# Kernel tuning notes

Measured on AMD Instinct MI355X. Metric: run time of the kernel, lower is better.

## Reference

```python
import jax, jax.numpy as jnp
import numpy as np

EPS = 1e-6

def _rmsnorm(x, w):
    # matches RMSNorm: compute in fp32, cast back, then scale by weight
    dt = x.dtype
    xf = x.astype(jnp.float32)
    var = jnp.mean(xf * xf, axis=-1, keepdims=True)
    xf = xf * jax.lax.rsqrt(var + EPS)
    return xf.astype(dt) * w


def setup_inputs() -> dict:
    key = jax.random.key(0)
    ks = jax.random.split(key, 4)
    B, N, C = 4, 2048, 1024
    H = 16
    D = C // H
    x = jax.random.normal(ks[0], (B, N, C), dtype=jnp.float32)
    W_qkv = jax.random.normal(ks[1], (C, 3 * C), dtype=jnp.float32) * (1.0 / np.sqrt(C))
    b_qkv = jnp.zeros((3 * C,), dtype=jnp.float32)
    W_proj = jax.random.normal(ks[2], (C, C), dtype=jnp.float32) * (1.0 / np.sqrt(C))
    b_proj = jnp.zeros((C,), dtype=jnp.float32)
    qn_w = jnp.ones((D,), dtype=jnp.float32)
    kn_w = jnp.ones((D,), dtype=jnp.float32)
    return {"x": x, "W_qkv": W_qkv, "b_qkv": b_qkv, "W_proj": W_proj,
            "b_proj": b_proj, "qn_w": qn_w, "kn_w": kn_w}


def reference(x, W_qkv, b_qkv, W_proj, b_proj, qn_w, kn_w):
    B, N, C = x.shape
    H = 16
    D = C // H
    qkv = jnp.einsum('bnc,cd->bnd', x, W_qkv) + b_qkv          # [B,N,3C]
    qkv = qkv.reshape(B, N, 3, H, D)
    q = qkv[:, :, 0].transpose(0, 2, 1, 3)                     # [B,H,N,D]
    k = qkv[:, :, 1].transpose(0, 2, 1, 3)
    v = qkv[:, :, 2].transpose(0, 2, 1, 3)
    q = _rmsnorm(q, qn_w)
    k = _rmsnorm(k, kn_w)
    scale = D ** -0.5
    attn = jnp.einsum('bhqd,bhkd->bhqk', q, k) * scale         # [B,H,N,N]
    attn = jax.nn.softmax(attn, axis=-1)
    out = jnp.einsum('bhqk,bhkd->bhqd', attn, v)               # [B,H,N,D]
    out = out.transpose(0, 2, 1, 3).reshape(B, N, C)
    out = jnp.einsum('bnc,cd->bnd', out, W_proj) + b_proj
    return out
```

## Files before the change

kernel.cpp:

```cpp
#include <hip/hip_runtime.h>
#include <stdint.h>

#define B_ 4
#define N_ 2048
#define C_ 1024
#define H_ 16
#define D_ 64
#define M_ (B_*N_)
#define N3_ (3*C_)

typedef __attribute__((ext_vector_type(8))) __bf16 bf16x8;
typedef bf16x8 bf16x8_ma __attribute__((may_alias));
typedef __attribute__((ext_vector_type(4))) float floatx4;
typedef unsigned short u16;
typedef unsigned int u32;

typedef __attribute__((address_space(1))) const void void_g;
typedef __attribute__((address_space(3))) void void_l;

__device__ __forceinline__ void glds16(const void* g, void* l) {
  __builtin_amdgcn_global_load_lds((void_g*)g, (void_l*)l, 16, 0, 0);
}

__device__ __forceinline__ u16 f2bf(float f) {
  union { float f; u32 u; } x; x.f = f;
  u32 r = x.u + 0x7fffu + ((x.u >> 16) & 1u);
  return (u16)(r >> 16);
}

__device__ __forceinline__ float fexp2(float x) {
#if __has_builtin(__builtin_amdgcn_exp2f)
  return __builtin_amdgcn_exp2f(x);
#else
  return exp2f(x);
#endif
}

__global__ __launch_bounds__(256)
void convert_x(const float4* __restrict__ in, uint2* __restrict__ out, int n4) {
  int idx = blockIdx.x * 256 + threadIdx.x;
  if (idx >= n4) return;
  float4 v = in[idx];
  union { u16 a[4]; uint2 u; } p;
  p.a[0] = f2bf(v.x); p.a[1] = f2bf(v.y); p.a[2] = f2bf(v.z); p.a[3] = f2bf(v.w);
  out[idx] = p.u;
}

__global__ __launch_bounds__(256)
void transpose_cvt(const float* __restrict__ in, u16* __restrict__ out,
                   int R, int Ccols) {
  __shared__ u16 tile[64][65];
  int c0 = blockIdx.x * 64, r0 = blockIdx.y * 64;
  int tid = threadIdx.x;
#pragma unroll
  for (int it = 0; it < 16; ++it) {
    int idx = it * 256 + tid;
    int r = idx >> 6, c = idx & 63;
    tile[c][r] = f2bf(in[(size_t)(r0 + r) * Ccols + c0 + c]);
  }
  __syncthreads();
#pragma unroll
  for (int it = 0; it < 16; ++it) {
    int idx = it * 256 + tid;
    int oc = idx >> 6, orr = idx & 63;
    out[(size_t)(c0 + oc) * R + r0 + orr] = tile[oc][orr];
  }
}

__global__ __launch_bounds__(256)
void transpose_v(const u16* __restrict__ qkv, u16* __restrict__ vt) {
  __shared__ u16 tile[64][65];
  int bh = blockIdx.y, b = bh >> 4, h = bh & 15;
  int n0 = blockIdx.x * 64;
  int tid = threadIdx.x;
#pragma unroll
  for (int it = 0; it < 16; ++it) {
    int idx = it * 256 + tid;
    int n = idx >> 6, d = idx & 63;
    tile[d][n] = qkv[(size_t)(b * N_ + n0 + n) * N3_ + 2 * C_ + h * D_ + d];
  }
  __syncthreads();
#pragma unroll
  for (int it = 0; it < 16; ++it) {
    int idx = it * 256 + tid;
    int d = idx >> 6, n = idx & 63;
    int np = (n & 0x23) | ((n & 0x0C) << 1) | ((n & 0x10) >> 2);
    vt[(size_t)(bh * D_ + d) * N_ + n0 + np] = tile[d][n];
  }
}

__global__ __launch_bounds__(256)
void gemm_bt(const u16* __restrict__ A, const u16* __restrict__ Bt,
             const float* __restrict__ bias, void* __restrict__ Cout,
             int Ncols, int lda, int do_rms, int out_fp32,
             const float* __restrict__ qn, const float* __restrict__ kn) {
  __shared__ __align__(16) u16 sA[8 * 512];
  __shared__ __align__(16) u16 sB[8 * 512];
  const int K = C_;
  int tid = threadIdx.x;
  int wave = tid >> 6, lane = tid & 63;
  int lrow = lane & 15, lq = lane >> 4;
  int n0 = blockIdx.x * 128;
  int m0 = blockIdx.y * 128;
  int wm = wave >> 1, wn = wave & 1;

  floatx4 acc[4][4];
#pragma unroll
  for (int i = 0; i < 4; ++i)
#pragma unroll
    for (int j = 0; j < 4; ++j) acc[i][j] = (floatx4){0.f, 0.f, 0.f, 0.f};

  const u16* ga0 = A  + (size_t)(m0 + (2 * wave + 0) * 16 + lrow) * lda + lq * 8;
  const u16* ga1 = A  + (size_t)(m0 + (2 * wave + 1) * 16 + lrow) * lda + lq * 8;
  const u16* gb0 = Bt + (size_t)(n0 + (2 * wave + 0) * 16 + lrow) * K + lq * 8;
  const u16* gb1 = Bt + (size_t)(n0 + (2 * wave + 1) * 16 + lrow) * K + lq * 8;
  u16* la0 = sA + (2 * wave + 0) * 512;
  u16* la1 = sA + (2 * wave + 1) * 512;
  u16* lb0 = sB + (2 * wave + 0) * 512;
  u16* lb1 = sB + (2 * wave + 1) * 512;

  for (int kt = 0; kt < K; kt += 32) {
    glds16(ga0 + kt, la0);
    glds16(ga1 + kt, la1);
    glds16(gb0 + kt, lb0);
    glds16(gb1 + kt, lb1);
    __syncthreads();
    bf16x8 af[4], bfr[4];
#pragma unroll
    for (int i = 0; i < 4; ++i)
      af[i] = *(const bf16x8_ma*)(sA + (wm * 4 + i) * 512 + lane * 8);
#pragma unroll
    for (int j = 0; j < 4; ++j)
      bfr[j] = *(const bf16x8_ma*)(sB + (wn * 4 + j) * 512 + lane * 8);
#pragma unroll
    for (int i = 0; i < 4; ++i)
#pragma unroll
      for (int j = 0; j < 4; ++j)
        acc[i][j] = __builtin_amdgcn_mfma_f32_16x16x32_bf16(af[i], bfr[j], acc[i][j], 0, 0, 0);
    __syncthreads();
  }

  int colbase = n0 + wn * 64;
  float bv[4];
#pragma unroll
  for (int j = 0; j < 4; ++j) bv[j] = bias[colbase + j * 16 + lrow];
#pragma unroll
  for (int i = 0; i < 4; ++i)
#pragma unroll
    for (int j = 0; j < 4; ++j)
#pragma unroll
      for (int r = 0; r < 4; ++r) acc[i][j][r] += bv[j];

  int sect = colbase >> 10;
  if (do_rms && sect < 2) {
    const float* wptr = (sect == 0) ? qn : kn;
    float wv[4];
#pragma unroll
    for (int j = 0; j < 4; ++j) wv[j] = wptr[j * 16 + lrow];
#pragma unroll
    for (int i = 0; i < 4; ++i)
#pragma unroll
      for (int r = 0; r < 4; ++r) {
        float ss = 0.f;
#pragma unroll
        for (int j = 0; j < 4; ++j) { float v = acc[i][j][r]; ss += v * v; }
        ss += __shfl_xor(ss, 1);
        ss += __shfl_xor(ss, 2);
        ss += __shfl_xor(ss, 4);
        ss += __shfl_xor(ss, 8);
        float rstd = rsqrtf(ss * (1.0f / 64.0f) + 1e-6f);
#pragma unroll
        for (int j = 0; j < 4; ++j) acc[i][j][r] *= rstd * wv[j];
      }
  }

#pragma unroll
  for (int i = 0; i < 4; ++i)
#pragma unroll
    for (int j = 0; j < 4; ++j)
#pragma unroll
      for (int r = 0; r < 4; ++r) {
        int row = m0 + wm * 64 + i * 16 + lq * 4 + r;
        int col = colbase + j * 16 + lrow;
        if (out_fp32)
          ((float*)Cout)[(size_t)row * Ncols + col] = acc[i][j][r];
        else
          ((u16*)Cout)[(size_t)row * Ncols + col] = f2bf(acc[i][j][r]);
      }
}

__global__ __launch_bounds__(256)
void flash_attn(u16* __restrict__ qkv, const u16* __restrict__ vt) {
  __shared__ __align__(16) u16 sK[8 * 512];
  __shared__ __align__(16) u16 sV[8 * 512];
  int tid = threadIdx.x;
  int wave = tid >> 6, lane = tid & 63;
  int lrow = lane & 15, lq = lane >> 4;
  int bh = blockIdx.y, b = bh >> 4, h = bh & 15;
  int q0 = blockIdx.x * 128;
  const float cc = 0.125f * 1.44269504088896340736f;
  const float co = 8.5f * 1.44269504088896340736f;

  bf16x8 qf[2][2];
#pragma unroll
  for (int i = 0; i < 2; ++i)
#pragma unroll
    for (int kq = 0; kq < 2; ++kq)
      qf[i][kq] = *(const bf16x8_ma*)(qkv +
          (size_t)(b * N_ + q0 + wave * 32 + i * 16 + lrow) * N3_ +
          h * D_ + kq * 32 + lq * 8);

  floatx4 aco[2][4];
#pragma unroll
  for (int i = 0; i < 2; ++i)
#pragma unroll
    for (int nd = 0; nd < 4; ++nd) aco[i][nd] = (floatx4){0.f, 0.f, 0.f, 0.f};
  float lsum[2] = {0.f, 0.f};

  for (int kt = 0; kt < 32; ++kt) {
    int key0 = kt * 64;
#pragma unroll
    for (int t = 0; t < 2; ++t) {
      int blk = wave * 2 + t;
      int j = blk >> 1, kq = blk & 1;
      const u16* g = qkv + (size_t)(b * N_ + key0 + j * 16 + lrow) * N3_ +
                     C_ + h * D_ + kq * 32 + lq * 8;
      glds16(g, sK + blk * 512);
    }
#pragma unroll
    for (int t = 0; t < 2; ++t) {
      int blk = wave * 2 + t;
      int nd = blk >> 1, kq = blk & 1;
      const u16* g = vt + (size_t)(bh * D_ + nd * 16 + lrow) * N_ +
                     key0 + kq * 32 + lq * 8;
      glds16(g, sV + blk * 512);
    }
    __syncthreads();

    floatx4 accs[2][4];
#pragma unroll
    for (int j = 0; j < 4; ++j) {
      bf16x8 kf0 = *(const bf16x8_ma*)(sK + (j * 2 + 0) * 512 + lane * 8);
      bf16x8 kf1 = *(const bf16x8_ma*)(sK + (j * 2 + 1) * 512 + lane * 8);
#pragma unroll
      for (int i = 0; i < 2; ++i) {
        floatx4 s = (floatx4){0.f, 0.f, 0.f, 0.f};
        s = __builtin_amdgcn_mfma_f32_16x16x32_bf16(kf0, qf[i][0], s, 0, 0, 0);
        s = __builtin_amdgcn_mfma_f32_16x16x32_bf16(kf1, qf[i][1], s, 0, 0, 0);
        accs[i][j] = s;
      }
    }

    bf16x8 pf[2][2];
#pragma unroll
    for (int i = 0; i < 2; ++i) {
      union { bf16x8 v; __bf16 e[8]; } pk0, pk1;
      float ls = 0.f;
#pragma unroll
      for (int j = 0; j < 4; ++j)
#pragma unroll
        for (int r = 0; r < 4; ++r) {
          float p = fexp2(fmaf(accs[i][j][r], cc, -co));
          ls += p;
          if (j < 2) pk0.e[(j & 1) * 4 + r] = (__bf16)p;
          else       pk1.e[(j & 1) * 4 + r] = (__bf16)p;
        }
      lsum[i] += ls;
      pf[i][0] = pk0.v;
      pf[i][1] = pk1.v;
    }

#pragma unroll
    for (int kq = 0; kq < 2; ++kq)
#pragma unroll
      for (int nd = 0; nd < 4; ++nd) {
        bf16x8 vf = *(const bf16x8_ma*)(sV + (nd * 2 + kq) * 512 + lane * 8);
        aco[0][nd] = __builtin_amdgcn_mfma_f32_16x16x32_bf16(vf, pf[0][kq], aco[0][nd], 0, 0, 0);
        aco[1][nd] = __builtin_amdgcn_mfma_f32_16x16x32_bf16(vf, pf[1][kq], aco[1][nd], 0, 0, 0);
      }
    __syncthreads();
  }

#pragma unroll
  for (int i = 0; i < 2; ++i) {
    float l = lsum[i];
    l += __shfl_xor(l, 16);
    l += __shfl_xor(l, 32);
    float inv = 1.0f / l;
    int row = q0 + wave * 32 + i * 16 + lrow;
#pragma unroll
    for (int nd = 0; nd < 4; ++nd) {
      union { u16 a[4]; uint2 u; } st;
#pragma unroll
      for (int r = 0; r < 4; ++r) st.a[r] = f2bf(aco[i][nd][r] * inv);
      *(uint2*)(qkv + (size_t)(b * N_ + row) * N3_ + h * D_ + nd * 16 + lq * 4) = st.u;
    }
  }
}

extern "C" void kernel_launch(void* const* d_in, const int* in_sizes, int n_in,
                              void* d_out, int out_size, void* d_ws, size_t ws_size,
                              hipStream_t stream) {
  (void)in_sizes; (void)n_in; (void)out_size; (void)ws_size;
  const float* x     = (const float*)d_in[0];
  const float* Wqkv  = (const float*)d_in[1];
  const float* bqkv  = (const float*)d_in[2];
  const float* Wproj = (const float*)d_in[3];
  const float* bproj = (const float*)d_in[4];
  const float* qn    = (const float*)d_in[5];
  const float* kn    = (const float*)d_in[6];
  float* out = (float*)d_out;

  char* ws = (char*)d_ws;
  u16* xb      = (u16*)ws;  ws += (size_t)M_ * C_ * 2;
  u16* Wt_qkv  = (u16*)ws;  ws += (size_t)N3_ * C_ * 2;
  u16* Wt_proj = (u16*)ws;  ws += (size_t)C_ * C_ * 2;
  u16* qkv     = (u16*)ws;  ws += (size_t)M_ * N3_ * 2;
  u16* vt      = (u16*)ws;  ws += (size_t)B_ * H_ * D_ * N_ * 2;

  convert_x<<<dim3(M_ * C_ / 4 / 256), 256, 0, stream>>>(
      (const float4*)x, (uint2*)xb, M_ * C_ / 4);
  transpose_cvt<<<dim3(N3_ / 64, C_ / 64), 256, 0, stream>>>(Wqkv, Wt_qkv, C_, N3_);
  transpose_cvt<<<dim3(C_ / 64, C_ / 64), 256, 0, stream>>>(Wproj, Wt_proj, C_, C_);
  gemm_bt<<<dim3(N3_ / 128, M_ / 128), 256, 0, stream>>>(
      xb, Wt_qkv, bqkv, qkv, N3_, C_, 1, 0, qn, kn);
  transpose_v<<<dim3(N_ / 64, B_ * H_), 256, 0, stream>>>(qkv, vt);
  flash_attn<<<dim3(N_ / 128, B_ * H_), 256, 0, stream>>>(qkv, vt);
  gemm_bt<<<dim3(C_ / 128, M_ / 128), 256, 0, stream>>>(
      qkv, Wt_proj, bproj, out, C_, N3_, 0, 1, qn, kn);
}
```

Measured before the change: 362.0 us.

## Double-buffer K/V tiles in flash attention and compute row sums via MFMA

```diff
diff --git a/kernel.cpp b/kernel.cpp
--- a/kernel.cpp
+++ b/kernel.cpp
@@ -191,8 +191,8 @@
 
 __global__ __launch_bounds__(256)
 void flash_attn(u16* __restrict__ qkv, const u16* __restrict__ vt) {
-  __shared__ __align__(16) u16 sK[8 * 512];
-  __shared__ __align__(16) u16 sV[8 * 512];
+  __shared__ __align__(16) u16 sK[2][8 * 512];
+  __shared__ __align__(16) u16 sV[2][8 * 512];
   int tid = threadIdx.x;
   int wave = tid >> 6, lane = tid & 63;
   int lrow = lane & 15, lq = lane >> 4;
@@ -210,38 +210,59 @@
           (size_t)(b * N_ + q0 + wave * 32 + i * 16 + lrow) * N3_ +
           h * D_ + kq * 32 + lq * 8);
 
+  union { bf16x8 v; u16 e[8]; } one_;
+#pragma unroll
+  for (int e = 0; e < 8; ++e) one_.e[e] = 0x3F80;
+  bf16x8 onef = one_.v;
+
   floatx4 aco[2][4];
-#pragma unroll
-  for (int i = 0; i < 2; ++i)
+  floatx4 acl[2];
+#pragma unroll
+  for (int i = 0; i < 2; ++i) {
 #pragma unroll
     for (int nd = 0; nd < 4; ++nd) aco[i][nd] = (floatx4){0.f, 0.f, 0.f, 0.f};
-  float lsum[2] = {0.f, 0.f};
+    acl[i] = (floatx4){0.f, 0.f, 0.f, 0.f};
+  }
+
+  const u16* gk[2];
+  const u16* gv[2];
+#pragma unroll
+  for (int t = 0; t < 2; ++t) {
+    int blk = wave * 2 + t;
+    int j = blk >> 1, kq = blk & 1;
+    gk[t] = qkv + (size_t)(b * N_ + j * 16 + lrow) * N3_ +
+            C_ + h * D_ + kq * 32 + lq * 8;
+    gv[t] = vt + (size_t)(bh * D_ + j * 16 + lrow) * N_ + kq * 32 + lq * 8;
+  }
+
+  u16* k_cur = &sK[0][0]; u16* k_nxt = &sK[1][0];
+  u16* v_cur = &sV[0][0]; u16* v_nxt = &sV[1][0];
+
+#pragma unroll
+  for (int t = 0; t < 2; ++t) {
+    int blk = wave * 2 + t;
+    glds16(gk[t], k_cur + blk * 512);
+    glds16(gv[t], v_cur + blk * 512);
+  }
+  __syncthreads();
 
   for (int kt = 0; kt < 32; ++kt) {
-    int key0 = kt * 64;
-#pragma unroll
-    for (int t = 0; t < 2; ++t) {
-      int blk = wave * 2 + t;
-      int j = blk >> 1, kq = blk & 1;
-      const u16* g = qkv + (size_t)(b * N_ + key0 + j * 16 + lrow) * N3_ +
-                     C_ + h * D_ + kq * 32 + lq * 8;
-      glds16(g, sK + blk * 512);
-    }
-#pragma unroll
-    for (int t = 0; t < 2; ++t) {
-      int blk = wave * 2 + t;
-      int nd = blk >> 1, kq = blk & 1;
-      const u16* g = vt + (size_t)(bh * D_ + nd * 16 + lrow) * N_ +
-                     key0 + kq * 32 + lq * 8;
-      glds16(g, sV + blk * 512);
-    }
-    __syncthreads();
+    if (kt < 31) {
+      size_t key0n = (size_t)(kt + 1) * 64;
+#pragma unroll
+      for (int t = 0; t < 2; ++t) {
+        int blk = wave * 2 + t;
+        glds16(gk[t] + key0n * N3_, k_nxt + blk * 512);
+        glds16(gv[t] + key0n, v_nxt + blk * 512);
+      }
+    }
 
     floatx4 accs[2][4];
+    __builtin_amdgcn_s_setprio(1);
 #pragma unroll
     for (int j = 0; j < 4; ++j) {
-      bf16x8 kf0 = *(const bf16x8_ma*)(sK + (j * 2 + 0) * 512 + lane * 8);
-      bf16x8 kf1 = *(const bf16x8_ma*)(sK + (j * 2 + 1) * 512 + lane * 8);
+      bf16x8 kf0 = *(const bf16x8_ma*)(k_cur + (j * 2 + 0) * 512 + lane * 8);
+      bf16x8 kf1 = *(const bf16x8_ma*)(k_cur + (j * 2 + 1) * 512 + lane * 8);
 #pragma unroll
       for (int i = 0; i < 2; ++i) {
         floatx4 s = (floatx4){0.f, 0.f, 0.f, 0.f};
@@ -250,43 +271,46 @@
         accs[i][j] = s;
       }
     }
+    __builtin_amdgcn_s_setprio(0);
 
     bf16x8 pf[2][2];
 #pragma unroll
     for (int i = 0; i < 2; ++i) {
       union { bf16x8 v; __bf16 e[8]; } pk0, pk1;
-      float ls = 0.f;
 #pragma unroll
       for (int j = 0; j < 4; ++j)
 #pragma unroll
         for (int r = 0; r < 4; ++r) {
           float p = fexp2(fmaf(accs[i][j][r], cc, -co));
-          ls += p;
           if (j < 2) pk0.e[(j & 1) * 4 + r] = (__bf16)p;
           else       pk1.e[(j & 1) * 4 + r] = (__bf16)p;
         }
-      lsum[i] += ls;
       pf[i][0] = pk0.v;
       pf[i][1] = pk1.v;
     }
 
-#pragma unroll
-    for (int kq = 0; kq < 2; ++kq)
+    __builtin_amdgcn_s_setprio(1);
+#pragma unroll
+    for (int kq = 0; kq < 2; ++kq) {
 #pragma unroll
       for (int nd = 0; nd < 4; ++nd) {
-        bf16x8 vf = *(const bf16x8_ma*)(sV + (nd * 2 + kq) * 512 + lane * 8);
+        bf16x8 vf = *(const bf16x8_ma*)(v_cur + (nd * 2 + kq) * 512 + lane * 8);
         aco[0][nd] = __builtin_amdgcn_mfma_f32_16x16x32_bf16(vf, pf[0][kq], aco[0][nd], 0, 0, 0);
         aco[1][nd] = __builtin_amdgcn_mfma_f32_16x16x32_bf16(vf, pf[1][kq], aco[1][nd], 0, 0, 0);
       }
+      acl[0] = __builtin_amdgcn_mfma_f32_16x16x32_bf16(onef, pf[0][kq], acl[0], 0, 0, 0);
+      acl[1] = __builtin_amdgcn_mfma_f32_16x16x32_bf16(onef, pf[1][kq], acl[1], 0, 0, 0);
+    }
+    __builtin_amdgcn_s_setprio(0);
+
     __syncthreads();
+    u16* t0 = k_cur; k_cur = k_nxt; k_nxt = t0;
+    u16* t1 = v_cur; v_cur = v_nxt; v_nxt = t1;
   }
 
 #pragma unroll
   for (int i = 0; i < 2; ++i) {
-    float l = lsum[i];
-    l += __shfl_xor(l, 16);
-    l += __shfl_xor(l, 32);
-    float inv = 1.0f / l;
+    float inv = 1.0f / acl[i][0];
     int row = q0 + wave * 32 + i * 16 + lrow;
 #pragma unroll
     for (int nd = 0; nd < 4; ++nd) {
```

Result: faster. 349.2 us (-3.5%).
